# Kernel optimization log

Measured on AMD Instinct MI355X. Metric: run time of the kernel, lower is better.

The kernel has to match this reference:

```python
import jax, jax.numpy as jnp
import numpy as np

C = 256
RED = 8
CK = C // RED  # 32


def setup_inputs() -> dict:
    key = jax.random.key(0)
    ks = jax.random.split(key, 7)
    x = jax.random.normal(ks[0], (4, C, 64, 64), dtype=jnp.float32)
    s = 1.0 / np.sqrt(C)
    key_W = jax.random.uniform(ks[1], (CK, C), minval=-s, maxval=s, dtype=jnp.float32)
    key_b = jax.random.uniform(ks[2], (CK,), minval=-s, maxval=s, dtype=jnp.float32)
    query_W = jax.random.uniform(ks[3], (CK, C), minval=-s, maxval=s, dtype=jnp.float32)
    query_b = jax.random.uniform(ks[4], (CK,), minval=-s, maxval=s, dtype=jnp.float32)
    value_W = jax.random.uniform(ks[5], (C, C), minval=-s, maxval=s, dtype=jnp.float32)
    value_b = jax.random.uniform(ks[6], (C,), minval=-s, maxval=s, dtype=jnp.float32)
    alpha = jnp.zeros((1,), dtype=jnp.float32)
    return {"x": x, "key_W": key_W, "key_b": key_b, "query_W": query_W,
            "query_b": query_b, "value_W": value_W, "value_b": value_b,
            "alpha": alpha}


def reference(x, key_W, key_b, query_W, query_b, value_W, value_b, alpha):
    B, Cc, H, W = x.shape
    N = H * W
    xf = x.reshape(B, Cc, N)  # [B, C, N]
    # 1x1 convs == per-pixel linear projections
    k = jnp.einsum('kc,bcn->bkn', key_W, xf) + key_b[None, :, None]     # [B, CK, N]
    q = jnp.einsum('kc,bcn->bkn', query_W, xf) + query_b[None, :, None]  # [B, CK, N]
    v = jnp.einsum('oc,bcn->bon', value_W, xf) + value_b[None, :, None]  # [B, C, N]
    # energy[b, i, j] = key_i . query_j
    energy = jnp.einsum('bki,bkj->bij', k, q)  # [B, N, N]
    attn = jax.nn.softmax(energy, axis=-1)
    # out[b, c, i] = sum_j v[b, c, j] * attn[b, i, j]
    out = jnp.einsum('bcj,bij->bci', v, attn)  # [B, C, N]
    out = out.reshape(B, Cc, H, W)
    return alpha * out + x
```

## Files before the change

### kernel.cpp

```cpp
#include <hip/hip_runtime.h>

#define C_DIM 256
#define CK_DIM 32
#define NPIX 4096
#define BATCH 4

typedef __attribute__((ext_vector_type(8))) short bf16x8;
typedef __attribute__((ext_vector_type(4))) float f32x4;
typedef __attribute__((ext_vector_type(16))) float f32x16;
typedef __attribute__((ext_vector_type(4))) unsigned short us4;

__device__ __forceinline__ unsigned short f2bf(float f) {
    union { float f; unsigned int u; } c; c.f = f;
    unsigned int r = c.u + 0x7FFFu + ((c.u >> 16) & 1u);
    return (unsigned short)(r >> 16);
}

__global__ __launch_bounds__(256) void wprep_kernel(
    const float* __restrict__ kW, const float* __restrict__ qW,
    const float* __restrict__ vW, unsigned short* __restrict__ wbf)
{
    int i4 = (blockIdx.x * 256 + threadIdx.x) * 4;
    int o = i4 >> 8, c = i4 & 255;
    const float* src = (o < 32) ? kW + o * 256 + c
                     : (o < 64) ? qW + (o - 32) * 256 + c
                                : vW + (o - 64) * 256 + c;
    float4 f = *(const float4*)src;
    us4 p; p.x = f2bf(f.x); p.y = f2bf(f.y); p.z = f2bf(f.z); p.w = f2bf(f.w);
    *(us4*)&wbf[i4] = p;
}

#define XP 264
__global__ __launch_bounds__(256) void proj_kernel(
    const float* __restrict__ x,
    const unsigned short* __restrict__ wbf,
    const float* __restrict__ key_b, const float* __restrict__ query_b,
    const float* __restrict__ value_b,
    unsigned short* __restrict__ kT,
    unsigned short* __restrict__ qT,
    unsigned short* __restrict__ vt)
{
    const int b  = blockIdx.y;
    const int n0 = blockIdx.x * 32;
    const int t  = threadIdx.x;
    const int w    = t >> 6;
    const int lane = t & 63;
    const int mrow = lane & 15;
    const int quad = lane >> 4;
    const int oh   = w >> 1;
    const int ns   = (w & 1) * 16;

    __shared__ __align__(16) unsigned short smem[14592];
    #define XT(n, c)       smem[(n) * XP + (c)]
    #define VS(nsb, c, nn) smem[(nsb) * 6144 + (c) * 24 + (nn)]
    #define KQS(n, o)      smem[12288 + (n) * 72 + (o)]

    const float* xb = x + (size_t)b * C_DIM * NPIX + n0;
    const int cb = (t >> 3) * 4;
    const int n4 = (t & 7) * 4;
    #pragma unroll
    for (int it = 0; it < 2; ++it) {
        int c0 = it * 128 + cb;
        float4 r0 = *(const float4*)(xb + (size_t)(c0 + 0) * NPIX + n4);
        float4 r1 = *(const float4*)(xb + (size_t)(c0 + 1) * NPIX + n4);
        float4 r2 = *(const float4*)(xb + (size_t)(c0 + 2) * NPIX + n4);
        float4 r3 = *(const float4*)(xb + (size_t)(c0 + 3) * NPIX + n4);
        float d0[4] = {r0.x, r0.y, r0.z, r0.w};
        float d1[4] = {r1.x, r1.y, r1.z, r1.w};
        float d2[4] = {r2.x, r2.y, r2.z, r2.w};
        float d3[4] = {r3.x, r3.y, r3.z, r3.w};
        #pragma unroll
        for (int d = 0; d < 4; ++d) {
            us4 p; p.x = f2bf(d0[d]); p.y = f2bf(d1[d]);
                   p.z = f2bf(d2[d]); p.w = f2bf(d3[d]);
            *(us4*)&XT(n4 + d, c0) = p;
        }
    }
    __syncthreads();

    f32x4 acc[10];
    #pragma unroll
    for (int ot = 0; ot < 10; ++ot) acc[ot] = (f32x4){0.f, 0.f, 0.f, 0.f};
    const int obase = oh * 160;
    const unsigned short* wp = wbf + (size_t)(obase + mrow) * 256 + quad * 8;

    bf16x8 awc[10], awn[10];
    #pragma unroll
    for (int ot = 0; ot < 10; ++ot)
        awc[ot] = *(const bf16x8*)(wp + (size_t)ot * 16 * 256);

    #pragma unroll
    for (int ck = 0; ck < 256; ck += 32) {
        bf16x8 bx = *(const bf16x8*)&XT(ns + mrow, ck + quad * 8);
        if (ck < 224) {
            #pragma unroll
            for (int ot = 0; ot < 10; ++ot)
                awn[ot] = *(const bf16x8*)(wp + (size_t)ot * 16 * 256 + ck + 32);
        }
        #pragma unroll
        for (int ot = 0; ot < 10; ++ot)
            acc[ot] = __builtin_amdgcn_mfma_f32_16x16x32_bf16(awc[ot], bx, acc[ot], 0, 0, 0);
        #pragma unroll
        for (int ot = 0; ot < 10; ++ot) awc[ot] = awn[ot];
    }
    __syncthreads();

    #pragma unroll
    for (int ot = 0; ot < 10; ++ot) {
        #pragma unroll
        for (int r = 0; r < 4; ++r) {
            int o = obase + 16 * ot + 4 * quad + r;
            float bias = (o < 32) ? key_b[o] : (o < 64) ? query_b[o - 32] : value_b[o - 64];
            unsigned short val = f2bf(acc[ot][r] + bias);
            if (o < 64) KQS(ns + mrow, o) = val;
            else        VS(ns >> 4, o - 64, mrow) = val;
        }
    }
    __syncthreads();

    {
        int n = t >> 3, o4 = (t & 7) * 4;
        *(us4*)&kT[((size_t)b * NPIX + n0 + n) * CK_DIM + o4] = *(const us4*)&KQS(n, o4);
        *(us4*)&qT[((size_t)b * NPIX + n0 + n) * CK_DIM + o4] = *(const us4*)&KQS(n, 32 + o4);
    }
    #pragma unroll
    for (int it = 0; it < 8; ++it) {
        int flat = it * 256 + t;
        int nsb = flat >> 10, c = (flat >> 2) & 255, nn = (flat & 3) * 4;
        unsigned short* vbase = vt + ((size_t)b * (NPIX / 16) + n0 / 16 + nsb) * (C_DIM * 16);
        *(us4*)&vbase[c * 16 + nn] = *(const us4*)&VS(nsb, c, nn);
    }
    #undef XT
    #undef VS
    #undef KQS
}

__global__ __launch_bounds__(512) void attn_kernel(
    const unsigned short* __restrict__ kT,
    const unsigned short* __restrict__ qT,
    const unsigned short* __restrict__ vt,
    const float* __restrict__ x, const float* __restrict__ alpha,
    float* __restrict__ out)
{
    const int f  = blockIdx.x;
    const int b  = (f & 7) >> 1;
    const int i0 = ((f >> 3) * 2 + (f & 1)) * 64;
    const int t  = threadIdx.x;
    const int w    = t >> 6;
    const int lane = t & 63;
    const int mrow = lane & 15;
    const int quad = lane >> 4;
    const int m32  = lane & 31;
    const int half = lane >> 5;

    __shared__ __align__(16) unsigned short Pt[2][64][136];
    __shared__ float lred[4][64];

    const unsigned short* kTb = kT + (size_t)b * NPIX * CK_DIM;
    const unsigned short* qTb = qT + (size_t)b * NPIX * CK_DIM;
    const unsigned short* vtb = vt + (size_t)b * (NPIX / 16) * (C_DIM * 16);

    int pp = 0;

    if (w < 4) {
        const int pw = w;
        bf16x8 kf[4];
        #pragma unroll
        for (int is = 0; is < 4; ++is)
            kf[is] = *(const bf16x8*)(kTb + (size_t)(i0 + 16 * is + mrow) * CK_DIM + quad * 8);

        float lacc[4] = {0.f, 0.f, 0.f, 0.f};

        #pragma unroll
        for (int js = 0; js < 2; ++js) {
            bf16x8 aq = *(const bf16x8*)(qTb + (size_t)(32 * pw + 16 * js + mrow) * CK_DIM + quad * 8);
            #pragma unroll
            for (int is = 0; is < 4; ++is) {
                f32x4 d = __builtin_amdgcn_mfma_f32_16x16x32_bf16(
                    aq, kf[is], (f32x4){0.f, 0.f, 0.f, 0.f}, 0, 0, 0);
                float p0 = __expf(d[0]), p1 = __expf(d[1]);
                float p2 = __expf(d[2]), p3 = __expf(d[3]);
                lacc[is] += (p0 + p1) + (p2 + p3);
                us4 p; p.x = f2bf(p0); p.y = f2bf(p1); p.z = f2bf(p2); p.w = f2bf(p3);
                *(us4*)&Pt[0][16 * is + mrow][32 * pw + 16 * js + 4 * quad] = p;
            }
        }
        bf16x8 aqc[2];
        #pragma unroll
        for (int js = 0; js < 2; ++js)
            aqc[js] = *(const bf16x8*)(qTb + (size_t)(128 + 32 * pw + 16 * js + mrow) * CK_DIM + quad * 8);

        __syncthreads();

        for (int jt = 0; jt < NPIX; jt += 128) {
            bf16x8 aqn[2];
            int jpre = (jt + 256) & (NPIX - 1);
            #pragma unroll
            for (int js = 0; js < 2; ++js)
                aqn[js] = *(const bf16x8*)(qTb + (size_t)(jpre + 32 * pw + 16 * js + mrow) * CK_DIM + quad * 8);

            if (jt + 128 < NPIX) {
                #pragma unroll
                for (int js = 0; js < 2; ++js) {
                    #pragma unroll
                    for (int is = 0; is < 4; ++is) {
                        f32x4 d = __builtin_amdgcn_mfma_f32_16x16x32_bf16(
                            aqc[js], kf[is], (f32x4){0.f, 0.f, 0.f, 0.f}, 0, 0, 0);
                        float p0 = __expf(d[0]), p1 = __expf(d[1]);
                        float p2 = __expf(d[2]), p3 = __expf(d[3]);
                        lacc[is] += (p0 + p1) + (p2 + p3);
                        us4 p; p.x = f2bf(p0); p.y = f2bf(p1); p.z = f2bf(p2); p.w = f2bf(p3);
                        *(us4*)&Pt[pp ^ 1][16 * is + mrow][32 * pw + 16 * js + 4 * quad] = p;
                    }
                }
            }
            aqc[0] = aqn[0]; aqc[1] = aqn[1];
            __syncthreads();
            pp ^= 1;
        }

        #pragma unroll
        for (int is = 0; is < 4; ++is) {
            lacc[is] += __shfl_xor(lacc[is], 16);
            lacc[is] += __shfl_xor(lacc[is], 32);
        }
        if (lane < 16) {
            #pragma unroll
            for (int is = 0; is < 4; ++is) lred[pw][16 * is + lane] = lacc[is];
        }
        __syncthreads();
    } else {
        const int cw = w - 4;
        const int c0 = cw * 64;

        f32x16 acc[2][2];
        #pragma unroll
        for (int cs = 0; cs < 2; ++cs)
            #pragma unroll
            for (int ih = 0; ih < 2; ++ih)
                #pragma unroll
                for (int r = 0; r < 16; ++r) acc[cs][ih][r] = 0.0f;

        bf16x8 av[8][2];
        #pragma unroll
        for (int jb = 0; jb < 8; ++jb) {
            const unsigned short* vp = vtb + (size_t)jb * (C_DIM * 16)
                                       + (size_t)(c0 + m32) * 16 + half * 8;
            av[jb][0] = *(const bf16x8*)vp;
            av[jb][1] = *(const bf16x8*)(vp + 32 * 16);
        }
        __syncthreads();

        for (int jt = 0; jt < NPIX; jt += 128) {
            #pragma unroll
            for (int jb = 0; jb < 8; ++jb) {
                bf16x8 bp0 = *(const bf16x8*)&Pt[pp][m32][16 * jb + half * 8];
                bf16x8 bp1 = *(const bf16x8*)&Pt[pp][32 + m32][16 * jb + half * 8];
                acc[0][0] = __builtin_amdgcn_mfma_f32_32x32x16_bf16(av[jb][0], bp0, acc[0][0], 0, 0, 0);
                acc[1][0] = __builtin_amdgcn_mfma_f32_32x32x16_bf16(av[jb][1], bp0, acc[1][0], 0, 0, 0);
                acc[0][1] = __builtin_amdgcn_mfma_f32_32x32x16_bf16(av[jb][0], bp1, acc[0][1], 0, 0, 0);
                acc[1][1] = __builtin_amdgcn_mfma_f32_32x32x16_bf16(av[jb][1], bp1, acc[1][1], 0, 0, 0);
            }
            int jpre = (jt + 128) & (NPIX - 1);
            #pragma unroll
            for (int jb = 0; jb < 8; ++jb) {
                const unsigned short* vp = vtb + (size_t)(jpre / 16 + jb) * (C_DIM * 16)
                                           + (size_t)(c0 + m32) * 16 + half * 8;
                av[jb][0] = *(const bf16x8*)vp;
                av[jb][1] = *(const bf16x8*)(vp + 32 * 16);
            }
            __syncthreads();
            pp ^= 1;
        }
        __syncthreads();

        const float al = alpha[0];
        float rs[2];
        #pragma unroll
        for (int ih = 0; ih < 2; ++ih) {
            int li = 32 * ih + m32;
            float l = (lred[0][li] + lred[1][li]) + (lred[2][li] + lred[3][li]);
            rs[ih] = al / l;
        }

        const float* xb = x + (size_t)b * C_DIM * NPIX;
        float* ob = out + (size_t)b * C_DIM * NPIX;
        #pragma unroll
        for (int cs = 0; cs < 2; ++cs)
            #pragma unroll
            for (int ih = 0; ih < 2; ++ih) {
                int i = i0 + 32 * ih + m32;
                #pragma unroll
                for (int r = 0; r < 16; ++r) {
                    int c = c0 + 32 * cs + (r & 3) + 8 * (r >> 2) + 4 * half;
                    size_t idx = (size_t)c * NPIX + i;
                    ob[idx] = acc[cs][ih][r] * rs[ih] + xb[idx];
                }
            }
    }
}

extern "C" void kernel_launch(void* const* d_in, const int* in_sizes, int n_in,
                              void* d_out, int out_size, void* d_ws, size_t ws_size,
                              hipStream_t stream) {
    const float* x       = (const float*)d_in[0];
    const float* key_W   = (const float*)d_in[1];
    const float* key_b   = (const float*)d_in[2];
    const float* query_W = (const float*)d_in[3];
    const float* query_b = (const float*)d_in[4];
    const float* value_W = (const float*)d_in[5];
    const float* value_b = (const float*)d_in[6];
    const float* alpha   = (const float*)d_in[7];
    float* out = (float*)d_out;

    unsigned short* kT  = (unsigned short*)d_ws;
    unsigned short* qT  = kT + (size_t)BATCH * NPIX * CK_DIM;
    unsigned short* vt  = qT + (size_t)BATCH * NPIX * CK_DIM;
    unsigned short* wbf = vt + (size_t)BATCH * C_DIM * NPIX;

    wprep_kernel<<<80, 256, 0, stream>>>(key_W, query_W, value_W, wbf);

    dim3 gridA(NPIX / 32, BATCH);
    proj_kernel<<<gridA, 256, 0, stream>>>(x, wbf, key_b, query_b, value_b, kT, qT, vt);

    attn_kernel<<<256, 512, 0, stream>>>(kT, qT, vt, x, alpha, out);
}
```

Measured before the change: 150.6 us.

## Halve attention and projection tiles to double grid size, fold log2e into key weights

The attention kernel now processes 32 query rows per block instead of 64 and launches 512 blocks instead of 256. This gives more blocks per CU on a 256-CU device, but each block does fewer MFMAs per load of V and P tiles, so operand reuse drops. The projection kernel likewise handles 16 pixels per block with 4 waves each owning 80 output channels. The key weights and bias are prescaled by log2(e) so the softmax can use the hardware exp2 instruction instead of __expf.

```diff
diff --git a/kernel.cpp b/kernel.cpp
--- a/kernel.cpp
+++ b/kernel.cpp
@@ -4,6 +4,7 @@
 #define CK_DIM 32
 #define NPIX 4096
 #define BATCH 4
+#define LOG2E 1.4426950408889634f
 
 typedef __attribute__((ext_vector_type(8))) short bf16x8;
 typedef __attribute__((ext_vector_type(4))) float f32x4;
@@ -14,6 +15,14 @@
     union { float f; unsigned int u; } c; c.f = f;
     unsigned int r = c.u + 0x7FFFu + ((c.u >> 16) & 1u);
     return (unsigned short)(r >> 16);
+}
+
+__device__ __forceinline__ float fast_exp2(float x) {
+#if __has_builtin(__builtin_amdgcn_exp2f)
+    return __builtin_amdgcn_exp2f(x);
+#else
+    return exp2f(x);
+#endif
 }
 
 __global__ __launch_bounds__(256) void wprep_kernel(
@@ -25,12 +34,13 @@
     const float* src = (o < 32) ? kW + o * 256 + c
                      : (o < 64) ? qW + (o - 32) * 256 + c
                                 : vW + (o - 64) * 256 + c;
+    float s = (o < 32) ? LOG2E : 1.0f;
     float4 f = *(const float4*)src;
-    us4 p; p.x = f2bf(f.x); p.y = f2bf(f.y); p.z = f2bf(f.z); p.w = f2bf(f.w);
+    us4 p; p.x = f2bf(f.x * s); p.y = f2bf(f.y * s);
+           p.z = f2bf(f.z * s); p.w = f2bf(f.w * s);
     *(us4*)&wbf[i4] = p;
 }
 
-#define XP 264
 __global__ __launch_bounds__(256) void proj_kernel(
     const float* __restrict__ x,
     const unsigned short* __restrict__ wbf,
@@ -41,30 +51,26 @@
     unsigned short* __restrict__ vt)
 {
     const int b  = blockIdx.y;
-    const int n0 = blockIdx.x * 32;
+    const int n0 = blockIdx.x * 16;
     const int t  = threadIdx.x;
     const int w    = t >> 6;
     const int lane = t & 63;
     const int mrow = lane & 15;
     const int quad = lane >> 4;
-    const int oh   = w >> 1;
-    const int ns   = (w & 1) * 16;
-
-    __shared__ __align__(16) unsigned short smem[14592];
-    #define XT(n, c)       smem[(n) * XP + (c)]
-    #define VS(nsb, c, nn) smem[(nsb) * 6144 + (c) * 24 + (nn)]
-    #define KQS(n, o)      smem[12288 + (n) * 72 + (o)]
+
+    __shared__ __align__(16) unsigned short smem[7296];
+    #define XT(n, c)   smem[(n) * 264 + (c)]
+    #define KQS(n, o)  smem[(n) * 72 + (o)]
+    #define VS(c, nn)  smem[1152 + (c) * 24 + (nn)]
 
     const float* xb = x + (size_t)b * C_DIM * NPIX + n0;
-    const int cb = (t >> 3) * 4;
-    const int n4 = (t & 7) * 4;
-    #pragma unroll
-    for (int it = 0; it < 2; ++it) {
-        int c0 = it * 128 + cb;
-        float4 r0 = *(const float4*)(xb + (size_t)(c0 + 0) * NPIX + n4);
-        float4 r1 = *(const float4*)(xb + (size_t)(c0 + 1) * NPIX + n4);
-        float4 r2 = *(const float4*)(xb + (size_t)(c0 + 2) * NPIX + n4);
-        float4 r3 = *(const float4*)(xb + (size_t)(c0 + 3) * NPIX + n4);
+    {
+        const int px4 = (t & 3) * 4;
+        const int c0  = (t >> 2) * 4;
+        float4 r0 = *(const float4*)(xb + (size_t)(c0 + 0) * NPIX + px4);
+        float4 r1 = *(const float4*)(xb + (size_t)(c0 + 1) * NPIX + px4);
+        float4 r2 = *(const float4*)(xb + (size_t)(c0 + 2) * NPIX + px4);
+        float4 r3 = *(const float4*)(xb + (size_t)(c0 + 3) * NPIX + px4);
         float d0[4] = {r0.x, r0.y, r0.z, r0.w};
         float d1[4] = {r1.x, r1.y, r1.z, r1.w};
         float d2[4] = {r2.x, r2.y, r2.z, r2.w};
@@ -73,66 +79,71 @@
         for (int d = 0; d < 4; ++d) {
             us4 p; p.x = f2bf(d0[d]); p.y = f2bf(d1[d]);
                    p.z = f2bf(d2[d]); p.w = f2bf(d3[d]);
-            *(us4*)&XT(n4 + d, c0) = p;
+            *(us4*)&XT(px4 + d, c0) = p;
         }
     }
     __syncthreads();
 
-    f32x4 acc[10];
+    f32x4 acc[5];
     #pragma unroll
-    for (int ot = 0; ot < 10; ++ot) acc[ot] = (f32x4){0.f, 0.f, 0.f, 0.f};
-    const int obase = oh * 160;
+    for (int ot = 0; ot < 5; ++ot) acc[ot] = (f32x4){0.f, 0.f, 0.f, 0.f};
+    const int obase = w * 80;
     const unsigned short* wp = wbf + (size_t)(obase + mrow) * 256 + quad * 8;
 
-    bf16x8 awc[10], awn[10];
+    bf16x8 awc[5], awn[5];
     #pragma unroll
-    for (int ot = 0; ot < 10; ++ot)
+    for (int ot = 0; ot < 5; ++ot)
         awc[ot] = *(const bf16x8*)(wp + (size_t)ot * 16 * 256);
 
     #pragma unroll
     for (int ck = 0; ck < 256; ck += 32) {
-        bf16x8 bx = *(const bf16x8*)&XT(ns + mrow, ck + quad * 8);
+        bf16x8 bx = *(const bf16x8*)&XT(mrow, ck + quad * 8);
         if (ck < 224) {
             #pragma unroll
-            for (int ot = 0; ot < 10; ++ot)
+            for (int ot = 0; ot < 5; ++ot)
                 awn[ot] = *(const bf16x8*)(wp + (size_t)ot * 16 * 256 + ck + 32);
         }
         #pragma unroll
-        for (int ot = 0; ot < 10; ++ot)
+        for (int ot = 0; ot < 5; ++ot)
             acc[ot] = __builtin_amdgcn_mfma_f32_16x16x32_bf16(awc[ot], bx, acc[ot], 0, 0, 0);
         #pragma unroll
-        for (int ot = 0; ot < 10; ++ot) awc[ot] = awn[ot];
+        for (int ot = 0; ot < 5; ++ot) awc[ot] = awn[ot];
     }
     __syncthreads();
 
     #pragma unroll
-    for (int ot = 0; ot < 10; ++ot) {
+    for (int ot = 0; ot < 5; ++ot) {
         #pragma unroll
         for (int r = 0; r < 4; ++r) {
             int o = obase + 16 * ot + 4 * quad + r;
-            float bias = (o < 32) ? key_b[o] : (o < 64) ? query_b[o - 32] : value_b[o - 64];
+            float bias = (o < 32) ? key_b[o] * LOG2E
+                       : (o < 64) ? query_b[o - 32] : value_b[o - 64];
             unsigned short val = f2bf(acc[ot][r] + bias);
-            if (o < 64) KQS(ns + mrow, o) = val;
-            else        VS(ns >> 4, o - 64, mrow) = val;
+            if (o < 64) KQS(mrow, o) = val;
+            else        VS(o - 64, mrow) = val;
         }
     }
     __syncthreads();
 
     {
-        int n = t >> 3, o4 = (t & 7) * 4;
-        *(us4*)&kT[((size_t)b * NPIX + n0 + n) * CK_DIM + o4] = *(const us4*)&KQS(n, o4);
-        *(us4*)&qT[((size_t)b * NPIX + n0 + n) * CK_DIM + o4] = *(const us4*)&KQS(n, 32 + o4);
-    }
-    #pragma unroll
-    for (int it = 0; it < 8; ++it) {
-        int flat = it * 256 + t;
-        int nsb = flat >> 10, c = (flat >> 2) & 255, nn = (flat & 3) * 4;
-        unsigned short* vbase = vt + ((size_t)b * (NPIX / 16) + n0 / 16 + nsb) * (C_DIM * 16);
-        *(us4*)&vbase[c * 16 + nn] = *(const us4*)&VS(nsb, c, nn);
+        int n = t >> 4, o4 = (t & 15) * 4;
+        if (o4 < 32)
+            *(us4*)&kT[((size_t)b * NPIX + n0 + n) * CK_DIM + o4] = *(const us4*)&KQS(n, o4);
+        else
+            *(us4*)&qT[((size_t)b * NPIX + n0 + n) * CK_DIM + (o4 - 32)] = *(const us4*)&KQS(n, o4);
+    }
+    {
+        unsigned short* vbase = vt + ((size_t)b * (NPIX / 16) + n0 / 16) * (C_DIM * 16);
+        #pragma unroll
+        for (int it = 0; it < 4; ++it) {
+            int flat = it * 256 + t;
+            int c = flat >> 2, nn = (flat & 3) * 4;
+            *(us4*)&vbase[c * 16 + nn] = *(const us4*)&VS(c, nn);
+        }
     }
     #undef XT
+    #undef KQS
     #undef VS
-    #undef KQS
 }
 
 __global__ __launch_bounds__(512) void attn_kernel(
@@ -144,7 +155,7 @@
 {
     const int f  = blockIdx.x;
     const int b  = (f & 7) >> 1;
-    const int i0 = ((f >> 3) * 2 + (f & 1)) * 64;
+    const int i0 = ((f >> 3) * 2 + (f & 1)) * 32;
     const int t  = threadIdx.x;
     const int w    = t >> 6;
     const int lane = t & 63;
@@ -153,8 +164,8 @@
     const int m32  = lane & 31;
     const int half = lane >> 5;
 
-    __shared__ __align__(16) unsigned short Pt[2][64][136];
-    __shared__ float lred[4][64];
+    __shared__ __align__(16) unsigned short Pt[2][32][136];
+    __shared__ float lred[4][32];
 
     const unsigned short* kTb = kT + (size_t)b * NPIX * CK_DIM;
     const unsigned short* qTb = qT + (size_t)b * NPIX * CK_DIM;
@@ -164,22 +175,22 @@
 
     if (w < 4) {
         const int pw = w;
-        bf16x8 kf[4];
-        #pragma unroll
-        for (int is = 0; is < 4; ++is)
+        bf16x8 kf[2];
+        #pragma unroll
+        for (int is = 0; is < 2; ++is)
             kf[is] = *(const bf16x8*)(kTb + (size_t)(i0 + 16 * is + mrow) * CK_DIM + quad * 8);
 
-        float lacc[4] = {0.f, 0.f, 0.f, 0.f};
+        float lacc[2] = {0.f, 0.f};
 
         #pragma unroll
         for (int js = 0; js < 2; ++js) {
             bf16x8 aq = *(const bf16x8*)(qTb + (size_t)(32 * pw + 16 * js + mrow) * CK_DIM + quad * 8);
             #pragma unroll
-            for (int is = 0; is < 4; ++is) {
+            for (int is = 0; is < 2; ++is) {
                 f32x4 d = __builtin_amdgcn_mfma_f32_16x16x32_bf16(
                     aq, kf[is], (f32x4){0.f, 0.f, 0.f, 0.f}, 0, 0, 0);
-                float p0 = __expf(d[0]), p1 = __expf(d[1]);
-                float p2 = __expf(d[2]), p3 = __expf(d[3]);
+                float p0 = fast_exp2(d[0]), p1 = fast_exp2(d[1]);
+                float p2 = fast_exp2(d[2]), p3 = fast_exp2(d[3]);
                 lacc[is] += (p0 + p1) + (p2 + p3);
                 us4 p; p.x = f2bf(p0); p.y = f2bf(p1); p.z = f2bf(p2); p.w = f2bf(p3);
                 *(us4*)&Pt[0][16 * is + mrow][32 * pw + 16 * js + 4 * quad] = p;
@@ -203,11 +214,11 @@
                 #pragma unroll
                 for (int js = 0; js < 2; ++js) {
                     #pragma unroll
-                    for (int is = 0; is < 4; ++is) {
+                    for (int is = 0; is < 2; ++is) {
                         f32x4 d = __builtin_amdgcn_mfma_f32_16x16x32_bf16(
                             aqc[js], kf[is], (f32x4){0.f, 0.f, 0.f, 0.f}, 0, 0, 0);
-                        float p0 = __expf(d[0]), p1 = __expf(d[1]);
-                        float p2 = __expf(d[2]), p3 = __expf(d[3]);
+                        float p0 = fast_exp2(d[0]), p1 = fast_exp2(d[1]);
+                        float p2 = fast_exp2(d[2]), p3 = fast_exp2(d[3]);
                         lacc[is] += (p0 + p1) + (p2 + p3);
                         us4 p; p.x = f2bf(p0); p.y = f2bf(p1); p.z = f2bf(p2); p.w = f2bf(p3);
                         *(us4*)&Pt[pp ^ 1][16 * is + mrow][32 * pw + 16 * js + 4 * quad] = p;
@@ -220,26 +231,24 @@
         }
 
         #pragma unroll
-        for (int is = 0; is < 4; ++is) {
+        for (int is = 0; is < 2; ++is) {
             lacc[is] += __shfl_xor(lacc[is], 16);
             lacc[is] += __shfl_xor(lacc[is], 32);
         }
         if (lane < 16) {
             #pragma unroll
-            for (int is = 0; is < 4; ++is) lred[pw][16 * is + lane] = lacc[is];
+            for (int is = 0; is < 2; ++is) lred[pw][16 * is + lane] = lacc[is];
         }
         __syncthreads();
     } else {
         const int cw = w - 4;
         const int c0 = cw * 64;
 
-        f32x16 acc[2][2];
+        f32x16 acc[2];
         #pragma unroll
         for (int cs = 0; cs < 2; ++cs)
             #pragma unroll
-            for (int ih = 0; ih < 2; ++ih)
-                #pragma unroll
-                for (int r = 0; r < 16; ++r) acc[cs][ih][r] = 0.0f;
+            for (int r = 0; r < 16; ++r) acc[cs][r] = 0.0f;
 
         bf16x8 av[8][2];
         #pragma unroll
@@ -254,12 +263,9 @@
         for (int jt = 0; jt < NPIX; jt += 128) {
             #pragma unroll
             for (int jb = 0; jb < 8; ++jb) {
-                bf16x8 bp0 = *(const bf16x8*)&Pt[pp][m32][16 * jb + half * 8];
-                bf16x8 bp1 = *(const bf16x8*)&Pt[pp][32 + m32][16 * jb + half * 8];
-                acc[0][0] = __builtin_amdgcn_mfma_f32_32x32x16_bf16(av[jb][0], bp0, acc[0][0], 0, 0, 0);
-                acc[1][0] = __builtin_amdgcn_mfma_f32_32x32x16_bf16(av[jb][1], bp0, acc[1][0], 0, 0, 0);
-                acc[0][1] = __builtin_amdgcn_mfma_f32_32x32x16_bf16(av[jb][0], bp1, acc[0][1], 0, 0, 0);
-                acc[1][1] = __builtin_amdgcn_mfma_f32_32x32x16_bf16(av[jb][1], bp1, acc[1][1], 0, 0, 0);
+                bf16x8 bp = *(const bf16x8*)&Pt[pp][m32][16 * jb + half * 8];
+                acc[0] = __builtin_amdgcn_mfma_f32_32x32x16_bf16(av[jb][0], bp, acc[0], 0, 0, 0);
+                acc[1] = __builtin_amdgcn_mfma_f32_32x32x16_bf16(av[jb][1], bp, acc[1], 0, 0, 0);
             }
             int jpre = (jt + 128) & (NPIX - 1);
             #pragma unroll
@@ -275,27 +281,19 @@
         __syncthreads();
 
         const float al = alpha[0];
-        float rs[2];
-        #pragma unroll
-        for (int ih = 0; ih < 2; ++ih) {
-            int li = 32 * ih + m32;
-            float l = (lred[0][li] + lred[1][li]) + (lred[2][li] + lred[3][li]);
-            rs[ih] = al / l;
-        }
+        float l = (lred[0][m32] + lred[1][m32]) + (lred[2][m32] + lred[3][m32]);
+        float rs = al / l;
 
         const float* xb = x + (size_t)b * C_DIM * NPIX;
         float* ob = out + (size_t)b * C_DIM * NPIX;
+        const int i = i0 + m32;
         #pragma unroll
         for (int cs = 0; cs < 2; ++cs)
             #pragma unroll
-            for (int ih = 0; ih < 2; ++ih) {
-                int i = i0 + 32 * ih + m32;
-                #pragma unroll
-                for (int r = 0; r < 16; ++r) {
-                    int c = c0 + 32 * cs + (r & 3) + 8 * (r >> 2) + 4 * half;
-                    size_t idx = (size_t)c * NPIX + i;
-                    ob[idx] = acc[cs][ih][r] * rs[ih] + xb[idx];
-                }
+            for (int r = 0; r < 16; ++r) {
+                int c = c0 + 32 * cs + (r & 3) + 8 * (r >> 2) + 4 * half;
+                size_t idx = (size_t)c * NPIX + i;
+                ob[idx] = acc[cs][r] * rs + xb[idx];
             }
     }
 }
@@ -320,8 +318,8 @@
 
     wprep_kernel<<<80, 256, 0, stream>>>(key_W, query_W, value_W, wbf);
 
-    dim3 gridA(NPIX / 32, BATCH);
+    dim3 gridA(NPIX / 16, BATCH);
     proj_kernel<<<gridA, 256, 0, stream>>>(x, wbf, key_b, query_b, value_b, kT, qT, vt);
 
-    attn_kernel<<<256, 512, 0, stream>>>(kT, qT, vt, x, alpha, out);
-}
+    attn_kernel<<<512, 512, 0, stream>>>(kT, qT, vt, x, alpha, out);
+}
```

After: 160.4 us. 6.5% more time.
